# Performance work log

Measured on AMD Instinct MI355X. Metric: run time of the kernel, lower is better.

Reference implementation:

```python
import jax, jax.numpy as jnp
import numpy as np

H = 256; NH = 8; DH = H // NH; L = 2; B = 32; S = 512; FIN = 199; A = 4


def _ln(x, g, b):
    m = jnp.mean(x, -1, keepdims=True)
    v = jnp.mean((x - m) ** 2, -1, keepdims=True)
    return (x - m) / jnp.sqrt(v + 1e-5) * g + b


def _grn(x, fc1w, fc1b, fc2w, fc2b, gw, gb, ggw, ggb, lg, lb):
    # GatedResidualNetwork, input_dim == output_dim so no skip layer, no context
    h = jax.nn.elu(x @ fc1w + fc1b)
    h = jax.nn.elu(h @ fc2w + fc2b)
    g = (h @ gw + gb) * jax.nn.sigmoid(h @ ggw + ggb)  # GLU
    return _ln(g + x, lg, lb)


def _attn(h, wq, bq, wk, bk, wv, bv, wo, bo):
    b, s, _ = h.shape
    q = (h @ wq + bq).reshape(b, s, NH, DH)
    k = (h @ wk + bk).reshape(b, s, NH, DH)
    v = (h @ wv + bv).reshape(b, s, NH, DH)
    scores = jnp.einsum('bqhd,bkhd->bhqk', q, k) / jnp.sqrt(jnp.float32(DH))
    mask = jnp.triu(jnp.ones((s, s), dtype=bool), 1)  # causal: mask strictly-future
    scores = jnp.where(mask, -jnp.inf, scores)
    aw = jax.nn.softmax(scores, axis=-1)
    ctx = jnp.einsum('bhqk,bkhd->bqhd', aw, v).reshape(b, s, H)
    return ctx @ wo + bo, aw


def _pe(s, d):
    pos = jnp.arange(s, dtype=jnp.float32)[:, None]
    div = jnp.exp(jnp.arange(0, d, 2, dtype=jnp.float32) * (-jnp.log(10000.0) / d))
    pe = jnp.zeros((s, d), dtype=jnp.float32)
    pe = pe.at[:, 0::2].set(jnp.sin(pos * div)).at[:, 1::2].set(jnp.cos(pos * div))
    return pe


def setup_inputs():
    key = jax.random.key(0)
    ks = iter(jax.random.split(key, 80))
    def nrm(shape, sc=0.02):
        return (jax.random.normal(next(ks), shape) * sc).astype(jnp.float32)
    d = {}
    d['x'] = jax.random.normal(next(ks), (B, S, FIN), dtype=jnp.float32)
    d['time_features'] = jax.random.normal(next(ks), (B, S, 3), dtype=jnp.float32)
    d['fp_w'] = nrm((FIN, H)); d['fp_b'] = jnp.zeros((H,), jnp.float32)
    d['tp_w'] = nrm((3, H));   d['tp_b'] = jnp.zeros((H,), jnp.float32)
    d['ip_w'] = nrm((H, H));   d['ip_b'] = jnp.zeros((H,), jnp.float32)
    for nm in ['wq', 'wk', 'wv', 'wo']:
        d[nm] = nrm((L, H, H))
    for nm in ['bq', 'bk', 'bv', 'bo']:
        d[nm] = jnp.zeros((L, H), jnp.float32)
    d['ln_g'] = jnp.ones((L, H), jnp.float32); d['ln_b'] = jnp.zeros((L, H), jnp.float32)
    for nm in ['g_fc1w', 'g_fc2w', 'g_gw', 'g_ggw']:
        d[nm] = nrm((L, H, H))
    for nm in ['g_fc1b', 'g_fc2b', 'g_gb', 'g_ggb']:
        d[nm] = jnp.zeros((L, H), jnp.float32)
    d['g_lg'] = jnp.ones((L, H), jnp.float32); d['g_lb'] = jnp.zeros((L, H), jnp.float32)
    for nm in ['f_fc1w', 'f_fc2w', 'f_gw', 'f_ggw']:
        d[nm] = nrm((H, H))
    for nm in ['f_fc1b', 'f_fc2b', 'f_gb', 'f_ggb']:
        d[nm] = jnp.zeros((H,), jnp.float32)
    d['f_lg'] = jnp.ones((H,), jnp.float32); d['f_lb'] = jnp.zeros((H,), jnp.float32)
    d['out_w'] = nrm((H, A)); d['out_b'] = jnp.zeros((A,), jnp.float32)
    return d


def reference(x, time_features, fp_w, fp_b, tp_w, tp_b, ip_w, ip_b,
              wq, bq, wk, bk, wv, bv, wo, bo, ln_g, ln_b,
              g_fc1w, g_fc1b, g_fc2w, g_fc2b, g_gw, g_gb, g_ggw, g_ggb, g_lg, g_lb,
              f_fc1w, f_fc1b, f_fc2w, f_fc2b, f_gw, f_gb, f_ggw, f_ggb, f_lg, f_lb,
              out_w, out_b):
    s = x.shape[1]
    hidden = (x @ fp_w + fp_b) + (time_features @ tp_w + tp_b)
    hidden = hidden @ ip_w + ip_b
    hidden = hidden + _pe(s, H)[None]
    aw = None
    for i in range(L):
        ao, aw = _attn(hidden, wq[i], bq[i], wk[i], bk[i], wv[i], bv[i], wo[i], bo[i])
        hidden = _ln(hidden + ao, ln_g[i], ln_b[i])
        hidden = _grn(hidden, g_fc1w[i], g_fc1b[i], g_fc2w[i], g_fc2b[i],
                      g_gw[i], g_gb[i], g_ggw[i], g_ggb[i], g_lg[i], g_lb[i])
    hidden = _grn(hidden, f_fc1w, f_fc1b, f_fc2w, f_fc2b, f_gw, f_gb, f_ggw, f_ggb, f_lg, f_lb)
    final = hidden[:, -1, :]
    logits = final @ out_w + out_b  # [B, A], one column per target asset
    return (logits, aw)
```

## Files before the change

### kernel.cpp

```cpp
#include <hip/hip_runtime.h>
#include <math.h>
#include <cstddef>

#define H 256
#define NH 8
#define DH 32
#define LAYERS 2
#define BB 32
#define SS 512
#define FINDIM 199
#define AA 4
#define T_TOK (BB*SS)
#define KIN 224

typedef unsigned short u16;
typedef unsigned int u32;
typedef __attribute__((ext_vector_type(8))) short short8;
typedef __attribute__((ext_vector_type(4))) float f4;

__device__ __forceinline__ float b2f(u16 v){
  unsigned u = ((unsigned)v) << 16;
  return __builtin_bit_cast(float, u);
}
__device__ __forceinline__ u16 f2b(float f){
  unsigned u = __builtin_bit_cast(unsigned, f);
  unsigned r = (u + 0x7fffu + ((u >> 16) & 1u)) >> 16;
  return (u16)r;
}
__device__ __forceinline__ float wave_sum(float v){
  #pragma unroll
  for (int mk=1; mk<64; mk<<=1) v += __shfl_xor(v, mk, 64);
  return v;
}

#define GLD_LDS16(g, l) \
  __builtin_amdgcn_global_load_lds((const __attribute__((address_space(1))) void*)(g), \
                                   (__attribute__((address_space(3))) void*)(l), 16, 0, 0)

template<int KC, int WK>
__device__ __forceinline__ void stage_acc(
    const u16* Xl, int sx, const u16* __restrict__ Wt,
    int c0, int l16, int lq, f4 acc[2][2])
{
  #pragma unroll
  for (int mi=0;mi<2;mi++)
    #pragma unroll
    for (int ni=0;ni<2;ni++) acc[mi][ni] = (f4){0.f,0.f,0.f,0.f};
  #pragma unroll
  for (int kc=0;kc<KC;kc++){
    short8 af[2], bf[2];
    af[0] = *(const short8*)&Xl[(l16)*sx      + kc*32 + lq*8];
    af[1] = *(const short8*)&Xl[(16+l16)*sx   + kc*32 + lq*8];
    bf[0] = *(const short8*)(Wt + (size_t)(c0+l16)*WK    + kc*32 + lq*8);
    bf[1] = *(const short8*)(Wt + (size_t)(c0+16+l16)*WK + kc*32 + lq*8);
    #pragma unroll
    for (int mi=0;mi<2;mi++)
      #pragma unroll
      for (int ni=0;ni<2;ni++)
        acc[mi][ni] = __builtin_amdgcn_mfma_f32_16x16x32_bf16(af[mi], bf[ni], acc[mi][ni], 0,0,0);
  }
}

template<int DO_ELU>
__device__ __forceinline__ void stage_store(
    f4 acc[2][2], const float* __restrict__ bias,
    int c0, int l16, int lq, u16* Yl, int sy)
{
  #pragma unroll
  for (int ni=0;ni<2;ni++){
    int col = c0 + ni*16 + l16;
    float bc = bias[col];
    #pragma unroll
    for (int mi=0;mi<2;mi++){
      #pragma unroll
      for (int r=0;r<4;r++){
        int row = mi*16 + lq*4 + r;
        float v = acc[mi][ni][r] + bc;
        if (DO_ELU) v = v > 0.f ? v : expm1f(v);
        Yl[row*sy + col] = f2b(v);
      }
    }
  }
}

__device__ __forceinline__ void tile_load256(const u16* g, u16* Yl, int sy, int t){
  #pragma unroll
  for (int j=0;j<2;j++){
    int u = t + j*512;
    int row = u >> 5, cu = u & 31;
    *(short8*)&Yl[row*sy + cu*8] = *(const short8*)(g + (size_t)row*H + cu*8);
  }
}

__device__ __forceinline__ void tile_ln(
    const u16* Yl, int sy, const float* __restrict__ g, const float* __restrict__ b,
    u16* out, int t)
{
  int w = t >> 6, lane = t & 63;
  #pragma unroll
  for (int rr=0;rr<4;rr++){
    int row = w*4 + rr;
    float xv[4];
    #pragma unroll
    for (int j=0;j<4;j++) xv[j] = b2f(Yl[row*sy + lane*4 + j]);
    float s=0.f, ss=0.f;
    #pragma unroll
    for (int j=0;j<4;j++){ s += xv[j]; ss += xv[j]*xv[j]; }
    s = wave_sum(s); ss = wave_sum(ss);
    float mean = s * (1.0f/H);
    float var  = ss * (1.0f/H) - mean*mean;
    float rstd = rsqrtf(var + 1e-5f);
    ushort4 o;
    int col = lane*4;
    o.x = f2b((xv[0]-mean)*rstd*g[col+0] + b[col+0]);
    o.y = f2b((xv[1]-mean)*rstd*g[col+1] + b[col+1]);
    o.z = f2b((xv[2]-mean)*rstd*g[col+2] + b[col+2]);
    o.w = f2b((xv[3]-mean)*rstd*g[col+3] + b[col+3]);
    *(ushort4*)(out + (size_t)row*H + col) = o;
  }
}

struct WPtrs { const float* p[21]; };

__global__ __launch_bounds__(256) void wconv_kernel(WPtrs wp, u16* __restrict__ dst){
  __shared__ float tl[64][65];
  int mb = blockIdx.x >> 4, tile = blockIdx.x & 15;
  int k0 = (tile >> 2) * 64, n0 = (tile & 3) * 64;
  const float* src = wp.p[mb];
  int t = threadIdx.x;
  int r = t >> 4, cg = t & 15;
  #pragma unroll
  for (int p4=0;p4<4;p4++){
    f4 v = *(const f4*)(src + (size_t)(k0 + r + p4*16)*H + n0 + cg*4);
    tl[r+p4*16][cg*4+0]=v[0]; tl[r+p4*16][cg*4+1]=v[1];
    tl[r+p4*16][cg*4+2]=v[2]; tl[r+p4*16][cg*4+3]=v[3];
  }
  __syncthreads();
  u16* db = dst + (size_t)mb*H*H;
  #pragma unroll
  for (int p4=0;p4<4;p4++){
    int rn = r + p4*16;
    ushort4 o;
    o.x = f2b(tl[cg*4+0][rn]); o.y = f2b(tl[cg*4+1][rn]);
    o.z = f2b(tl[cg*4+2][rn]); o.w = f2b(tl[cg*4+3][rn]);
    *(ushort4*)(db + (size_t)(n0+rn)*H + k0 + cg*4) = o;
  }
}

__global__ __launch_bounds__(256) void wcat_kernel(
    const float* __restrict__ fp_w, const float* __restrict__ tp_w,
    u16* __restrict__ wcat){
  int idx = blockIdx.x*256 + threadIdx.x;
  if (idx >= 256*KIN) return;
  int n = idx / KIN, k2 = idx % KIN;
  float v = 0.f;
  if (k2 < FINDIM) v = fp_w[(size_t)k2*H + n];
  else if (k2 < FINDIM+3) v = tp_w[(size_t)(k2-FINDIM)*H + n];
  wcat[idx] = f2b(v);
}

__global__ __launch_bounds__(256) void xconv_kernel(
    const float* __restrict__ x, const float* __restrict__ tf,
    u16* __restrict__ ab){
  size_t idx = (size_t)blockIdx.x*256 + threadIdx.x;
  if (idx >= (size_t)T_TOK*KIN) return;
  int tok = idx / KIN, k2 = idx % KIN;
  float v = 0.f;
  if (k2 < FINDIM) v = x[(size_t)tok*FINDIM + k2];
  else if (k2 < FINDIM+3) v = tf[(size_t)tok*3 + (k2-FINDIM)];
  ab[idx] = f2b(v);
}

#define SA (KIN+8)
#define SY (H+8)

__global__ __launch_bounds__(512) void input_kernel(
    const u16* __restrict__ ab, const u16* __restrict__ wcat,
    const float* __restrict__ fp_b, const float* __restrict__ tp_b,
    const u16* __restrict__ ipw, const float* __restrict__ ip_b,
    u16* __restrict__ hid){
  __shared__ u16 Al[32*SA];
  __shared__ u16 Tl[32*SY];
  int t = threadIdx.x;
  int tok0 = blockIdx.x * 32;
  int lane = t & 63, w = t >> 6;
  int l16 = lane & 15, lq = lane >> 4;
  int c0 = w * 32;

  #pragma unroll
  for (int j=0;j<2;j++){
    int u = t + j*512;
    if (u < 896){
      int row = u / 28, cu = u % 28;
      *(short8*)&Al[row*SA + cu*8] = *(const short8*)(ab + (size_t)(tok0+row)*KIN + cu*8);
    }
  }
  __syncthreads();

  f4 acc[2][2];
  stage_acc<7, KIN>(Al, SA, wcat, c0, l16, lq, acc);
  #pragma unroll
  for (int ni=0;ni<2;ni++){
    int col = c0 + ni*16 + l16;
    float bc = fp_b[col] + tp_b[col];
    #pragma unroll
    for (int mi=0;mi<2;mi++)
      #pragma unroll
      for (int r=0;r<4;r++){
        int row = mi*16 + lq*4 + r;
        Tl[row*SY + col] = f2b(acc[mi][ni][r] + bc);
      }
  }
  __syncthreads();

  stage_acc<8, H>(Tl, SY, ipw, c0, l16, lq, acc);
  #pragma unroll
  for (int ni=0;ni<2;ni++){
    int col = c0 + ni*16 + l16;
    float bc = ip_b[col];
    int ii = col >> 1;
    float div = __expf((float)(2*ii) * -0.03597789207803197f);
    #pragma unroll
    for (int mi=0;mi<2;mi++)
      #pragma unroll
      for (int r=0;r<4;r++){
        int row = mi*16 + lq*4 + r;
        int s = (tok0 + row) & (SS-1);
        float arg = (float)s * div;
        float pe = (col & 1) ? cosf(arg) : sinf(arg);
        hid[(size_t)(tok0+row)*H + col] = f2b(acc[mi][ni][r] + bc + pe);
      }
  }
}

__global__ __launch_bounds__(512) void oproj_ln_kernel(
    const u16* __restrict__ ctx, u16* __restrict__ hid,
    const u16* __restrict__ wo, const float* __restrict__ bo,
    const float* __restrict__ g, const float* __restrict__ b){
  __shared__ u16 Xl[32*SY];
  __shared__ u16 Rl[32*SY];
  int t = threadIdx.x;
  int tok0 = blockIdx.x * 32;
  int lane = t & 63, w = t >> 6;
  int l16 = lane & 15, lq = lane >> 4;
  int c0 = w * 32;
  u16* hb = hid + (size_t)tok0*H;

  tile_load256(ctx + (size_t)tok0*H, Xl, SY, t);
  tile_load256(hb, Rl, SY, t);
  __syncthreads();

  f4 acc[2][2];
  stage_acc<8, H>(Xl, SY, wo, c0, l16, lq, acc);
  __syncthreads();
  #pragma unroll
  for (int ni=0;ni<2;ni++){
    int col = c0 + ni*16 + l16;
    float bc = bo[col];
    #pragma unroll
    for (int mi=0;mi<2;mi++)
      #pragma unroll
      for (int r=0;r<4;r++){
        int row = mi*16 + lq*4 + r;
        float y = acc[mi][ni][r] + bc + b2f(Rl[row*SY + col]);
        Xl[row*SY + col] = f2b(y);
      }
  }
  __syncthreads();
  tile_ln(Xl, SY, g, b, hb, t);
}

__global__ __launch_bounds__(512) void grn_kernel(
    u16* __restrict__ hid,
    const u16* __restrict__ fc1, const u16* __restrict__ fc2,
    const u16* __restrict__ gw,  const u16* __restrict__ ggw,
    const float* __restrict__ b1, const float* __restrict__ b2,
    const float* __restrict__ gb, const float* __restrict__ ggb,
    const float* __restrict__ lg, const float* __restrict__ lb){
  __shared__ u16 Xl[32*SY];
  __shared__ u16 H1[32*SY];
  __shared__ u16 H2[32*SY];
  int t = threadIdx.x;
  int tok0 = blockIdx.x * 32;
  int lane = t & 63, w = t >> 6;
  int l16 = lane & 15, lq = lane >> 4;
  int c0 = w * 32;
  u16* hb = hid + (size_t)tok0*H;

  tile_load256(hb, Xl, SY, t);
  __syncthreads();

  f4 acc[2][2];
  stage_acc<8, H>(Xl, SY, fc1, c0, l16, lq, acc);
  stage_store<1>(acc, b1, c0, l16, lq, H1, SY);
  __syncthreads();
  stage_acc<8, H>(H1, SY, fc2, c0, l16, lq, acc);
  stage_store<1>(acc, b2, c0, l16, lq, H2, SY);
  __syncthreads();
  stage_acc<8, H>(H2, SY, gw, c0, l16, lq, acc);
  stage_store<0>(acc, gb, c0, l16, lq, H1, SY);
  __syncthreads();
  stage_acc<8, H>(H2, SY, ggw, c0, l16, lq, acc);
  __syncthreads();
  #pragma unroll
  for (int ni=0;ni<2;ni++){
    int col = c0 + ni*16 + l16;
    float bc = ggb[col];
    #pragma unroll
    for (int mi=0;mi<2;mi++)
      #pragma unroll
      for (int r=0;r<4;r++){
        int row = mi*16 + lq*4 + r;
        float gg = acc[mi][ni][r] + bc;
        float sg = 1.0f/(1.0f + __expf(-gg));
        float y  = b2f(H1[row*SY + col]) * sg + b2f(Xl[row*SY + col]);
        H2[row*SY + col] = f2b(y);
      }
  }
  __syncthreads();
  tile_ln(H2, SY, lg, lb, hb, t);
}

struct GemmJob  { const u16* Wt; const float* bias; u16* C; };
struct GemmBatch{ GemmJob j[3]; };

__global__ __launch_bounds__(256) void gemm_bf16(
    const u16* __restrict__ A, GemmBatch jb) {
  __shared__ u16 smem[128*64 + 64*64];
  u16* As  = smem;
  u16* Wsm = smem + 128*64;
  const GemmJob job = jb.j[blockIdx.z];
  const u16* Wt = job.Wt;
  int t = threadIdx.x;
  int m0 = blockIdx.x * 128;
  int n0 = blockIdx.y * 64;
  int lane = t & 63, w = t >> 6;
  int wr = (w >> 1) * 64;
  int wc = (w & 1) * 32;
  int l16 = lane & 15, lq = lane >> 4;

  f4 acc[4][2];
  #pragma unroll
  for (int mi=0;mi<4;mi++)
    #pragma unroll
    for (int ni=0;ni<2;ni++) acc[mi][ni] = (f4){0.f,0.f,0.f,0.f};

  for (int k0=0;k0<256;k0+=64){
    #pragma unroll
    for (int ja=0;ja<4;ja++){
      int ub = (w*4 + ja)*64;
      int u  = ub + lane;
      int m  = u >> 3, c = u & 7, kx = c ^ (m & 7);
      const u16* g = A + (size_t)(m0+m)*H + k0 + kx*8;
      GLD_LDS16(g, As + (size_t)ub*8);
    }
    #pragma unroll
    for (int jb2=0;jb2<2;jb2++){
      int ub = (w*2 + jb2)*64;
      int u  = ub + lane;
      int n  = u >> 3, c = u & 7, kx = c ^ (n & 7);
      const u16* g = Wt + (size_t)(n0+n)*H + k0 + kx*8;
      GLD_LDS16(g, Wsm + (size_t)ub*8);
    }
    __syncthreads();
    #pragma unroll
    for (int kc=0;kc<2;kc++){
      short8 af[4], bf[2];
      int kx = kc*4 + lq;
      #pragma unroll
      for (int mi=0;mi<4;mi++){
        int m = wr + mi*16 + l16;
        int un = (m<<3) | (kx ^ (m&7));
        af[mi] = *(short8*)&As[un*8];
      }
      #pragma unroll
      for (int ni=0;ni<2;ni++){
        int n = wc + ni*16 + l16;
        int un = (n<<3) | (kx ^ (n&7));
        bf[ni] = *(short8*)&Wsm[un*8];
      }
      #pragma unroll
      for (int mi=0;mi<4;mi++)
        #pragma unroll
        for (int ni=0;ni<2;ni++)
          acc[mi][ni] = __builtin_amdgcn_mfma_f32_16x16x32_bf16(af[mi], bf[ni], acc[mi][ni], 0,0,0);
    }
    __syncthreads();
  }

  u16* Cl = smem;
  #pragma unroll
  for (int ni=0;ni<2;ni++){
    int coll = wc + ni*16 + l16;
    float bcol = job.bias[n0 + coll];
    #pragma unroll
    for (int mi=0;mi<4;mi++){
      #pragma unroll
      for (int r=0;r<4;r++){
        int rowl = wr + mi*16 + lq*4 + r;
        Cl[rowl*68 + coll] = f2b(acc[mi][ni][r] + bcol);
      }
    }
  }
  __syncthreads();
  #pragma unroll
  for (int q2=0;q2<4;q2++){
    int u = q2*256 + t;
    int row = u >> 3, cu = u & 7;
    short8 val = *(short8*)&Cl[row*68 + cu*8];
    *(short8*)(job.C + (size_t)(m0+row)*H + n0 + cu*8) = val;
  }
}

template<int WRITE_AW>
__global__ __launch_bounds__(256) void attn_kernel(
    const u16* __restrict__ q, const u16* __restrict__ k,
    const u16* __restrict__ v, float* __restrict__ aw,
    u16* __restrict__ ctx) {
  __shared__ u16 Vt[DH][SS+8];
  __shared__ u16 Plds[4][16][72];
  int t  = threadIdx.x;
  int zg = blockIdx.x;
  int bh = blockIdx.y;
  int b  = bh >> 3, h = bh & 7;
  int lane = t & 63, w = t >> 6;
  int l16 = lane & 15, lq = lane >> 4;
  const float scale = 0.17677669529663687f;

  #pragma unroll
  for (int rep=0;rep<2;rep++){
    int kk = t + rep*256;
    const u16* vp = v + ((size_t)(b*SS + kk))*H + h*DH;
    short8 r0 = *(const short8*)(vp);
    short8 r1 = *(const short8*)(vp+8);
    short8 r2 = *(const short8*)(vp+16);
    short8 r3 = *(const short8*)(vp+24);
    #pragma unroll
    for (int j=0;j<8;j++){
      Vt[j][kk]    = (u16)r0[j];
      Vt[8+j][kk]  = (u16)r1[j];
      Vt[16+j][kk] = (u16)r2[j];
      Vt[24+j][kk] = (u16)r3[j];
    }
  }
  __syncthreads();

  for (int it=0; it<4; it++){
    int qt  = zg + it*2;
    int qr0 = qt*64 + w*16;
    int KT  = qt*4 + w + 1;
    short8 af = *(const short8*)(q + ((size_t)(b*SS + qr0 + l16))*H + h*DH + lq*8);

    float l[4] = {0.f,0.f,0.f,0.f};
    f4 o[2] = {(f4){0.f,0.f,0.f,0.f}, (f4){0.f,0.f,0.f,0.f}};
    u32 pk0[32], pk1[32];

    #pragma unroll
    for (int c8=0;c8<8;c8++){
      if (c8*4 < KT){
        #pragma unroll
        for (int j=0;j<4;j++){
          int kt = c8*4 + j;
          float p[4] = {0.f,0.f,0.f,0.f};
          if (kt < KT){
            short8 bfr = *(const short8*)(k + ((size_t)(b*SS + kt*16 + l16))*H + h*DH + lq*8);
            f4 cc = (f4){0.f,0.f,0.f,0.f};
            cc = __builtin_amdgcn_mfma_f32_16x16x32_bf16(af, bfr, cc, 0,0,0);
            int col = kt*16 + l16;
            #pragma unroll
            for (int i=0;i<4;i++){
              int qi = qr0 + lq*4 + i;
              float sc = (col <= qi) ? cc[i]*scale : -3.0e38f;
              p[i] = __expf(sc);
              l[i] += p[i];
            }
          }
          u16 pb[4];
          #pragma unroll
          for (int i=0;i<4;i++) pb[i] = f2b(p[i]);
          if (WRITE_AW){
            pk0[kt] = (u32)pb[0] | ((u32)pb[1] << 16);
            pk1[kt] = (u32)pb[2] | ((u32)pb[3] << 16);
          }
          #pragma unroll
          for (int i=0;i<4;i++) Plds[w][lq*4+i][j*16+l16] = pb[i];
        }
        #pragma unroll
        for (int kc=0;kc<2;kc++){
          short8 pa = *(short8*)&Plds[w][l16][kc*32 + lq*8];
          #pragma unroll
          for (int dt=0;dt<2;dt++){
            short8 vb = *(const short8*)&Vt[dt*16 + l16][c8*64 + kc*32 + lq*8];
            o[dt] = __builtin_amdgcn_mfma_f32_16x16x32_bf16(pa, vb, o[dt], 0,0,0);
          }
        }
      }
    }

    #pragma unroll
    for (int i=0;i<4;i++){
      #pragma unroll
      for (int mk=1; mk<16; mk<<=1) l[i] += __shfl_xor(l[i], mk, 64);
    }
    float inv[4];
    #pragma unroll
    for (int i=0;i<4;i++) inv[i] = 1.0f / l[i];

    if (WRITE_AW){
      float* ab = aw + (size_t)bh*SS*SS;
      #pragma unroll
      for (int kt=0;kt<32;kt++){
        if (kt < KT){
          int col = kt*16 + l16;
          float pv[4] = { b2f((u16)pk0[kt]), b2f((u16)(pk0[kt]>>16)),
                          b2f((u16)pk1[kt]), b2f((u16)(pk1[kt]>>16)) };
          #pragma unroll
          for (int i=0;i<4;i++){
            int qi = qr0 + lq*4 + i;
            ab[(size_t)qi*SS + col] = (col <= qi) ? pv[i]*inv[i] : 0.f;
          }
        }
      }
      int c4base = KT*4;
      f4 z = (f4){0.f,0.f,0.f,0.f};
      #pragma unroll
      for (int ri=0;ri<4;ri++){
        int row = qr0 + ri*4 + lq;
        for (int j=l16; j < 128 - c4base; j += 16)
          *(f4*)&ab[(size_t)row*SS + (size_t)(c4base+j)*4] = z;
      }
    }

    #pragma unroll
    for (int dt=0;dt<2;dt++){
      #pragma unroll
      for (int i=0;i<4;i++){
        int row = qr0 + lq*4 + i;
        ctx[((size_t)(b*SS + row))*H + h*DH + dt*16 + l16] = f2b(o[dt][i]*inv[i]);
      }
    }
  }
}

__global__ __launch_bounds__(128) void logits_kernel(
    const u16* __restrict__ hid, const float* __restrict__ ow,
    const float* __restrict__ ob, float* __restrict__ out){
  int t = threadIdx.x;
  int b = t >> 2, a = t & 3;
  const u16* hr = hid + ((size_t)b*SS + (SS-1))*H;
  float acc = ob[a];
  for (int k2=0;k2<H;k2++) acc = fmaf(b2f(hr[k2]), ow[k2*AA + a], acc);
  out[t] = acc;
}

extern "C" void kernel_launch(void* const* d_in, const int* in_sizes, int n_in,
                              void* d_out, int out_size, void* d_ws, size_t ws_size,
                              hipStream_t stream){
  (void)in_sizes; (void)n_in; (void)out_size; (void)ws_size;
  const float* x      = (const float*)d_in[0];
  const float* tf     = (const float*)d_in[1];
  const float* fp_w   = (const float*)d_in[2];
  const float* fp_b   = (const float*)d_in[3];
  const float* tp_w   = (const float*)d_in[4];
  const float* tp_b   = (const float*)d_in[5];
  const float* ip_w   = (const float*)d_in[6];
  const float* ip_b   = (const float*)d_in[7];
  const float* wq     = (const float*)d_in[8];
  const float* wk     = (const float*)d_in[9];
  const float* wv     = (const float*)d_in[10];
  const float* wo     = (const float*)d_in[11];
  const float* bq     = (const float*)d_in[12];
  const float* bk     = (const float*)d_in[13];
  const float* bv     = (const float*)d_in[14];
  const float* bo     = (const float*)d_in[15];
  const float* ln_g   = (const float*)d_in[16];
  const float* ln_b   = (const float*)d_in[17];
  const float* g_fc1w = (const float*)d_in[18];
  const float* g_fc2w = (const float*)d_in[19];
  const float* g_gw   = (const float*)d_in[20];
  const float* g_ggw  = (const float*)d_in[21];
  const float* g_fc1b = (const float*)d_in[22];
  const float* g_fc2b = (const float*)d_in[23];
  const float* g_gb   = (const float*)d_in[24];
  const float* g_ggb  = (const float*)d_in[25];
  const float* g_lg   = (const float*)d_in[26];
  const float* g_lb   = (const float*)d_in[27];
  const float* f_fc1w = (const float*)d_in[28];
  const float* f_fc2w = (const float*)d_in[29];
  const float* f_gw   = (const float*)d_in[30];
  const float* f_ggw  = (const float*)d_in[31];
  const float* f_fc1b = (const float*)d_in[32];
  const float* f_fc2b = (const float*)d_in[33];
  const float* f_gb   = (const float*)d_in[34];
  const float* f_ggb  = (const float*)d_in[35];
  const float* f_lg   = (const float*)d_in[36];
  const float* f_lb   = (const float*)d_in[37];
  const float* out_w  = (const float*)d_in[38];
  const float* out_b  = (const float*)d_in[39];

  float* logits = (float*)d_out;
  float* aw     = logits + BB*AA;

  u16* wts = (u16*)d_ws;
  const size_t WMAT = (size_t)H*H;
  u16* wcat = wts  + 21*WMAT;
  u16* abuf = wcat + (size_t)H*KIN;
  u16* hid  = abuf + (size_t)T_TOK*KIN;
  size_t BUF = (size_t)T_TOK * H;
  u16* buf1 = hid  + BUF;
  u16* buf2 = buf1 + BUF;
  u16* buf3 = buf2 + BUF;

  WPtrs wp;
  wp.p[0]  = ip_w;
  wp.p[1]  = wq;        wp.p[2]  = wq + WMAT;
  wp.p[3]  = wk;        wp.p[4]  = wk + WMAT;
  wp.p[5]  = wv;        wp.p[6]  = wv + WMAT;
  wp.p[7]  = wo;        wp.p[8]  = wo + WMAT;
  wp.p[9]  = g_fc1w;    wp.p[10] = g_fc1w + WMAT;
  wp.p[11] = g_fc2w;    wp.p[12] = g_fc2w + WMAT;
  wp.p[13] = g_gw;      wp.p[14] = g_gw + WMAT;
  wp.p[15] = g_ggw;     wp.p[16] = g_ggw + WMAT;
  wp.p[17] = f_fc1w;    wp.p[18] = f_fc2w;
  wp.p[19] = f_gw;      wp.p[20] = f_ggw;
  const int WT_IP=0, WT_Q=1, WT_K=3, WT_V=5, WT_O=7,
            WT_FC1=9, WT_FC2=11, WT_GW=13, WT_GGW=15,
            WT_FFC1=17, WT_FFC2=18, WT_FGW=19, WT_FGGW=20;

  dim3 b256(256), b512(512);
  dim3 gAttn(2, BB*NH);
  dim3 gTok(T_TOK/32);

  wconv_kernel<<<21*16, b256, 0, stream>>>(wp, wts);
  wcat_kernel<<<(H*KIN+255)/256, b256, 0, stream>>>(fp_w, tp_w, wcat);
  xconv_kernel<<<(T_TOK*KIN+255)/256, b256, 0, stream>>>(x, tf, abuf);
  input_kernel<<<gTok, b512, 0, stream>>>(abuf, wcat, fp_b, tp_b,
                                          wts + (size_t)WT_IP*WMAT, ip_b, hid);

  for (int i=0;i<LAYERS;i++){
    const size_t BOFF = (size_t)i*H;
    GemmBatch gb;
    gb.j[0] = { wts + (size_t)(WT_Q+i)*WMAT, bq+BOFF, buf1 };
    gb.j[1] = { wts + (size_t)(WT_K+i)*WMAT, bk+BOFF, buf2 };
    gb.j[2] = { wts + (size_t)(WT_V+i)*WMAT, bv+BOFF, buf3 };
    gemm_bf16<<<dim3(T_TOK/128, H/64, 3), b256, 0, stream>>>(hid, gb);
    if (i == LAYERS-1)
      attn_kernel<1><<<gAttn, b256, 0, stream>>>(buf1, buf2, buf3, aw, buf1);
    else
      attn_kernel<0><<<gAttn, b256, 0, stream>>>(buf1, buf2, buf3, aw, buf1);
    oproj_ln_kernel<<<gTok, b512, 0, stream>>>(buf1, hid,
        wts + (size_t)(WT_O+i)*WMAT, bo+BOFF, ln_g+BOFF, ln_b+BOFF);
    grn_kernel<<<gTok, b512, 0, stream>>>(hid,
        wts + (size_t)(WT_FC1+i)*WMAT, wts + (size_t)(WT_FC2+i)*WMAT,
        wts + (size_t)(WT_GW+i)*WMAT,  wts + (size_t)(WT_GGW+i)*WMAT,
        g_fc1b+BOFF, g_fc2b+BOFF, g_gb+BOFF, g_ggb+BOFF,
        g_lg+BOFF, g_lb+BOFF);
  }

  grn_kernel<<<gTok, b512, 0, stream>>>(hid,
      wts + (size_t)WT_FFC1*WMAT, wts + (size_t)WT_FFC2*WMAT,
      wts + (size_t)WT_FGW*WMAT,  wts + (size_t)WT_FGGW*WMAT,
      f_fc1b, f_fc2b, f_gb, f_ggb, f_lg, f_lb);

  logits_kernel<<<1, 128, 0, stream>>>(hid, out_w, out_b, logits);
}
```

Before: 673.8 us.

## Use 64-token tiles in row-wise kernels and fuse logits into final GRN

Doubles the token tile in the input, o-proj+LN and GRN kernels to 64 rows, with each wave computing a 32x64 output block, so each weight fragment loaded from global memory feeds twice as many MFMAs. Shared memory is cut by reading residuals straight from global and holding the sigmoid gate in registers as packed fp16. The logits projection is folded into the last GRN kernel, and attention-weight stores become nontemporal. The trade-offs are higher register pressure with fewer blocks, and a small precision change from the fp16 gate.

```diff
diff --git a/kernel.cpp b/kernel.cpp
--- a/kernel.cpp
+++ b/kernel.cpp
@@ -1,4 +1,5 @@
 #include <hip/hip_runtime.h>
+#include <hip/hip_fp16.h>
 #include <math.h>
 #include <cstddef>
 
@@ -12,6 +13,7 @@
 #define AA 4
 #define T_TOK (BB*SS)
 #define KIN 224
+#define TPB 64
 
 typedef unsigned short u16;
 typedef unsigned int u32;
@@ -37,44 +39,49 @@
   __builtin_amdgcn_global_load_lds((const __attribute__((address_space(1))) void*)(g), \
                                    (__attribute__((address_space(3))) void*)(l), 16, 0, 0)
 
+#define SA (KIN+8)
+#define SY (H+8)
+
 template<int KC, int WK>
-__device__ __forceinline__ void stage_acc(
+__device__ __forceinline__ void stage_acc64(
     const u16* Xl, int sx, const u16* __restrict__ Wt,
-    int c0, int l16, int lq, f4 acc[2][2])
+    int r0, int c0, int l16, int lq, f4 acc[2][4])
 {
   #pragma unroll
   for (int mi=0;mi<2;mi++)
     #pragma unroll
-    for (int ni=0;ni<2;ni++) acc[mi][ni] = (f4){0.f,0.f,0.f,0.f};
+    for (int ni=0;ni<4;ni++) acc[mi][ni] = (f4){0.f,0.f,0.f,0.f};
   #pragma unroll
   for (int kc=0;kc<KC;kc++){
-    short8 af[2], bf[2];
-    af[0] = *(const short8*)&Xl[(l16)*sx      + kc*32 + lq*8];
-    af[1] = *(const short8*)&Xl[(16+l16)*sx   + kc*32 + lq*8];
-    bf[0] = *(const short8*)(Wt + (size_t)(c0+l16)*WK    + kc*32 + lq*8);
-    bf[1] = *(const short8*)(Wt + (size_t)(c0+16+l16)*WK + kc*32 + lq*8);
+    short8 af[2], bf[4];
     #pragma unroll
     for (int mi=0;mi<2;mi++)
-      #pragma unroll
-      for (int ni=0;ni<2;ni++)
+      af[mi] = *(const short8*)&Xl[(r0 + mi*16 + l16)*sx + kc*32 + lq*8];
+    #pragma unroll
+    for (int ni=0;ni<4;ni++)
+      bf[ni] = *(const short8*)(Wt + (size_t)(c0 + ni*16 + l16)*WK + kc*32 + lq*8);
+    #pragma unroll
+    for (int mi=0;mi<2;mi++)
+      #pragma unroll
+      for (int ni=0;ni<4;ni++)
         acc[mi][ni] = __builtin_amdgcn_mfma_f32_16x16x32_bf16(af[mi], bf[ni], acc[mi][ni], 0,0,0);
   }
 }
 
 template<int DO_ELU>
-__device__ __forceinline__ void stage_store(
-    f4 acc[2][2], const float* __restrict__ bias,
-    int c0, int l16, int lq, u16* Yl, int sy)
+__device__ __forceinline__ void stage_store64(
+    f4 acc[2][4], const float* __restrict__ bias,
+    int r0, int c0, int l16, int lq, u16* Yl, int sy)
 {
   #pragma unroll
-  for (int ni=0;ni<2;ni++){
+  for (int ni=0;ni<4;ni++){
     int col = c0 + ni*16 + l16;
     float bc = bias[col];
     #pragma unroll
     for (int mi=0;mi<2;mi++){
       #pragma unroll
       for (int r=0;r<4;r++){
-        int row = mi*16 + lq*4 + r;
+        int row = r0 + mi*16 + lq*4 + r;
         float v = acc[mi][ni][r] + bc;
         if (DO_ELU) v = v > 0.f ? v : expm1f(v);
         Yl[row*sy + col] = f2b(v);
@@ -83,23 +90,24 @@
   }
 }
 
-__device__ __forceinline__ void tile_load256(const u16* g, u16* Yl, int sy, int t){
-  #pragma unroll
-  for (int j=0;j<2;j++){
+__device__ __forceinline__ void tile_load64(const u16* g, u16* Yl, int sy, int t){
+  #pragma unroll
+  for (int j=0;j<4;j++){
     int u = t + j*512;
     int row = u >> 5, cu = u & 31;
     *(short8*)&Yl[row*sy + cu*8] = *(const short8*)(g + (size_t)row*H + cu*8);
   }
 }
 
-__device__ __forceinline__ void tile_ln(
-    const u16* Yl, int sy, const float* __restrict__ g, const float* __restrict__ b,
+template<int WB>
+__device__ __forceinline__ void tile_ln64(
+    u16* Yl, int sy, const float* __restrict__ g, const float* __restrict__ b,
     u16* out, int t)
 {
   int w = t >> 6, lane = t & 63;
   #pragma unroll
-  for (int rr=0;rr<4;rr++){
-    int row = w*4 + rr;
+  for (int rr=0;rr<8;rr++){
+    int row = w*8 + rr;
     float xv[4];
     #pragma unroll
     for (int j=0;j<4;j++) xv[j] = b2f(Yl[row*sy + lane*4 + j]);
@@ -117,6 +125,7 @@
     o.z = f2b((xv[2]-mean)*rstd*g[col+2] + b[col+2]);
     o.w = f2b((xv[3]-mean)*rstd*g[col+3] + b[col+3]);
     *(ushort4*)(out + (size_t)row*H + col) = o;
+    if (WB && row == 63) *(ushort4*)(Yl + row*sy + col) = o;
   }
 }
 
@@ -171,51 +180,49 @@
   ab[idx] = f2b(v);
 }
 
-#define SA (KIN+8)
-#define SY (H+8)
-
-__global__ __launch_bounds__(512) void input_kernel(
+__global__ __launch_bounds__(512,4) void input_kernel(
     const u16* __restrict__ ab, const u16* __restrict__ wcat,
     const float* __restrict__ fp_b, const float* __restrict__ tp_b,
     const u16* __restrict__ ipw, const float* __restrict__ ip_b,
     u16* __restrict__ hid){
-  __shared__ u16 Al[32*SA];
-  __shared__ u16 Tl[32*SY];
+  __shared__ u16 Al[TPB*SA];
+  __shared__ u16 Tl[TPB*SY];
   int t = threadIdx.x;
-  int tok0 = blockIdx.x * 32;
+  int tok0 = blockIdx.x * TPB;
   int lane = t & 63, w = t >> 6;
   int l16 = lane & 15, lq = lane >> 4;
-  int c0 = w * 32;
-
-  #pragma unroll
-  for (int j=0;j<2;j++){
+  int r0 = (w >> 2) * 32;
+  int c0 = (w & 3) * 64;
+
+  #pragma unroll
+  for (int j=0;j<4;j++){
     int u = t + j*512;
-    if (u < 896){
+    if (u < 1792){
       int row = u / 28, cu = u % 28;
       *(short8*)&Al[row*SA + cu*8] = *(const short8*)(ab + (size_t)(tok0+row)*KIN + cu*8);
     }
   }
   __syncthreads();
 
-  f4 acc[2][2];
-  stage_acc<7, KIN>(Al, SA, wcat, c0, l16, lq, acc);
-  #pragma unroll
-  for (int ni=0;ni<2;ni++){
+  f4 acc[2][4];
+  stage_acc64<7, KIN>(Al, SA, wcat, r0, c0, l16, lq, acc);
+  #pragma unroll
+  for (int ni=0;ni<4;ni++){
     int col = c0 + ni*16 + l16;
     float bc = fp_b[col] + tp_b[col];
     #pragma unroll
     for (int mi=0;mi<2;mi++)
       #pragma unroll
       for (int r=0;r<4;r++){
-        int row = mi*16 + lq*4 + r;
+        int row = r0 + mi*16 + lq*4 + r;
         Tl[row*SY + col] = f2b(acc[mi][ni][r] + bc);
       }
   }
   __syncthreads();
 
-  stage_acc<8, H>(Tl, SY, ipw, c0, l16, lq, acc);
-  #pragma unroll
-  for (int ni=0;ni<2;ni++){
+  stage_acc64<8, H>(Tl, SY, ipw, r0, c0, l16, lq, acc);
+  #pragma unroll
+  for (int ni=0;ni<4;ni++){
     int col = c0 + ni*16 + l16;
     float bc = ip_b[col];
     int ii = col >> 1;
@@ -224,7 +231,7 @@
     for (int mi=0;mi<2;mi++)
       #pragma unroll
       for (int r=0;r<4;r++){
-        int row = mi*16 + lq*4 + r;
+        int row = r0 + mi*16 + lq*4 + r;
         int s = (tok0 + row) & (SS-1);
         float arg = (float)s * div;
         float pe = (col & 1) ? cosf(arg) : sinf(arg);
@@ -233,92 +240,136 @@
   }
 }
 
-__global__ __launch_bounds__(512) void oproj_ln_kernel(
+__global__ __launch_bounds__(512,4) void oproj_ln_kernel(
     const u16* __restrict__ ctx, u16* __restrict__ hid,
     const u16* __restrict__ wo, const float* __restrict__ bo,
     const float* __restrict__ g, const float* __restrict__ b){
-  __shared__ u16 Xl[32*SY];
-  __shared__ u16 Rl[32*SY];
+  __shared__ u16 Xl[TPB*SY];
   int t = threadIdx.x;
-  int tok0 = blockIdx.x * 32;
+  int tok0 = blockIdx.x * TPB;
   int lane = t & 63, w = t >> 6;
   int l16 = lane & 15, lq = lane >> 4;
-  int c0 = w * 32;
+  int r0 = (w >> 2) * 32;
+  int c0 = (w & 3) * 64;
   u16* hb = hid + (size_t)tok0*H;
 
-  tile_load256(ctx + (size_t)tok0*H, Xl, SY, t);
-  tile_load256(hb, Rl, SY, t);
-  __syncthreads();
-
-  f4 acc[2][2];
-  stage_acc<8, H>(Xl, SY, wo, c0, l16, lq, acc);
-  __syncthreads();
-  #pragma unroll
-  for (int ni=0;ni<2;ni++){
+  tile_load64(ctx + (size_t)tok0*H, Xl, SY, t);
+  __syncthreads();
+
+  f4 acc[2][4];
+  stage_acc64<8, H>(Xl, SY, wo, r0, c0, l16, lq, acc);
+  __syncthreads();
+  #pragma unroll
+  for (int ni=0;ni<4;ni++){
     int col = c0 + ni*16 + l16;
     float bc = bo[col];
     #pragma unroll
     for (int mi=0;mi<2;mi++)
       #pragma unroll
       for (int r=0;r<4;r++){
-        int row = mi*16 + lq*4 + r;
-        float y = acc[mi][ni][r] + bc + b2f(Rl[row*SY + col]);
+        int row = r0 + mi*16 + lq*4 + r;
+        float y = acc[mi][ni][r] + bc + b2f(hb[(size_t)row*H + col]);
         Xl[row*SY + col] = f2b(y);
       }
   }
   __syncthreads();
-  tile_ln(Xl, SY, g, b, hb, t);
-}
-
-__global__ __launch_bounds__(512) void grn_kernel(
+  tile_ln64<0>(Xl, SY, g, b, hb, t);
+}
+
+template<int LOGITS>
+__global__ __launch_bounds__(512,4) void grn_kernel(
     u16* __restrict__ hid,
     const u16* __restrict__ fc1, const u16* __restrict__ fc2,
     const u16* __restrict__ gw,  const u16* __restrict__ ggw,
     const float* __restrict__ b1, const float* __restrict__ b2,
     const float* __restrict__ gb, const float* __restrict__ ggb,
-    const float* __restrict__ lg, const float* __restrict__ lb){
-  __shared__ u16 Xl[32*SY];
-  __shared__ u16 H1[32*SY];
-  __shared__ u16 H2[32*SY];
+    const float* __restrict__ lg, const float* __restrict__ lb,
+    const float* __restrict__ ow, const float* __restrict__ ob,
+    float* __restrict__ lout){
+  __shared__ u16 Xa[TPB*SY];
+  __shared__ u16 Xb[TPB*SY];
   int t = threadIdx.x;
-  int tok0 = blockIdx.x * 32;
+  int tok0 = blockIdx.x * TPB;
   int lane = t & 63, w = t >> 6;
   int l16 = lane & 15, lq = lane >> 4;
-  int c0 = w * 32;
+  int r0 = (w >> 2) * 32;
+  int c0 = (w & 3) * 64;
   u16* hb = hid + (size_t)tok0*H;
 
-  tile_load256(hb, Xl, SY, t);
-  __syncthreads();
-
-  f4 acc[2][2];
-  stage_acc<8, H>(Xl, SY, fc1, c0, l16, lq, acc);
-  stage_store<1>(acc, b1, c0, l16, lq, H1, SY);
-  __syncthreads();
-  stage_acc<8, H>(H1, SY, fc2, c0, l16, lq, acc);
-  stage_store<1>(acc, b2, c0, l16, lq, H2, SY);
-  __syncthreads();
-  stage_acc<8, H>(H2, SY, gw, c0, l16, lq, acc);
-  stage_store<0>(acc, gb, c0, l16, lq, H1, SY);
-  __syncthreads();
-  stage_acc<8, H>(H2, SY, ggw, c0, l16, lq, acc);
-  __syncthreads();
-  #pragma unroll
-  for (int ni=0;ni<2;ni++){
+  tile_load64(hb, Xa, SY, t);
+  __syncthreads();
+
+  f4 acc[2][4];
+  stage_acc64<8, H>(Xa, SY, fc1, r0, c0, l16, lq, acc);
+  stage_store64<1>(acc, b1, r0, c0, l16, lq, Xb, SY);
+  __syncthreads();
+  stage_acc64<8, H>(Xb, SY, fc2, r0, c0, l16, lq, acc);
+  stage_store64<1>(acc, b2, r0, c0, l16, lq, Xa, SY);
+  __syncthreads();
+
+  stage_acc64<8, H>(Xa, SY, ggw, r0, c0, l16, lq, acc);
+  u32 sgp[2][4][2];
+  #pragma unroll
+  for (int mi=0;mi<2;mi++)
+    #pragma unroll
+    for (int ni=0;ni<4;ni++){
+      float bc = ggb[c0 + ni*16 + l16];
+      float s0 = 1.0f/(1.0f + __expf(-(acc[mi][ni][0]+bc)));
+      float s1 = 1.0f/(1.0f + __expf(-(acc[mi][ni][1]+bc)));
+      float s2 = 1.0f/(1.0f + __expf(-(acc[mi][ni][2]+bc)));
+      float s3 = 1.0f/(1.0f + __expf(-(acc[mi][ni][3]+bc)));
+      sgp[mi][ni][0] = __builtin_bit_cast(u32, __floats2half2_rn(s0, s1));
+      sgp[mi][ni][1] = __builtin_bit_cast(u32, __floats2half2_rn(s2, s3));
+    }
+
+  stage_acc64<8, H>(Xa, SY, gw, r0, c0, l16, lq, acc);
+  #pragma unroll
+  for (int ni=0;ni<4;ni++){
     int col = c0 + ni*16 + l16;
-    float bc = ggb[col];
-    #pragma unroll
-    for (int mi=0;mi<2;mi++)
+    float bc = gb[col];
+    #pragma unroll
+    for (int mi=0;mi<2;mi++){
+      float2 s01 = __half22float2(__builtin_bit_cast(__half2, sgp[mi][ni][0]));
+      float2 s23 = __half22float2(__builtin_bit_cast(__half2, sgp[mi][ni][1]));
+      float sv[4] = {s01.x, s01.y, s23.x, s23.y};
       #pragma unroll
       for (int r=0;r<4;r++){
-        int row = mi*16 + lq*4 + r;
-        float gg = acc[mi][ni][r] + bc;
-        float sg = 1.0f/(1.0f + __expf(-gg));
-        float y  = b2f(H1[row*SY + col]) * sg + b2f(Xl[row*SY + col]);
-        H2[row*SY + col] = f2b(y);
-      }
-  }
-  __syncthreads();
-  tile_ln(H2, SY, lg, lb, hb, t);
+        int row = r0 + mi*16 + lq*4 + r;
+        float y = (acc[mi][ni][r] + bc) * sv[r] + b2f(hb[(size_t)row*H + col]);
+        Xb[row*SY + col] = f2b(y);
+      }
+    }
+  }
+  __syncthreads();
+  tile_ln64<LOGITS>(Xb, SY, lg, lb, hb, t);
+
+  if (LOGITS){
+    if ((tok0 & (SS-1)) == SS - TPB){
+      __syncthreads();
+      if (t < 64){
+        int bidx = tok0 >> 9;
+        float a0=0.f, a1=0.f, a2=0.f, a3=0.f;
+        #pragma unroll
+        for (int j=0;j<4;j++){
+          int k = t*4 + j;
+          float xv = b2f(Xb[63*SY + k]);
+          f4 wr = *(const f4*)(ow + (size_t)k*AA);
+          a0 = fmaf(xv, wr[0], a0);
+          a1 = fmaf(xv, wr[1], a1);
+          a2 = fmaf(xv, wr[2], a2);
+          a3 = fmaf(xv, wr[3], a3);
+        }
+        a0 = wave_sum(a0); a1 = wave_sum(a1);
+        a2 = wave_sum(a2); a3 = wave_sum(a3);
+        if (t == 0){
+          lout[bidx*AA+0] = a0 + ob[0];
+          lout[bidx*AA+1] = a1 + ob[1];
+          lout[bidx*AA+2] = a2 + ob[2];
+          lout[bidx*AA+3] = a3 + ob[3];
+        }
+      }
+    }
+  }
 }
 
 struct GemmJob  { const u16* Wt; const float* bias; u16* C; };
@@ -517,7 +568,8 @@
           #pragma unroll
           for (int i=0;i<4;i++){
             int qi = qr0 + lq*4 + i;
-            ab[(size_t)qi*SS + col] = (col <= qi) ? pv[i]*inv[i] : 0.f;
+            float val = (col <= qi) ? pv[i]*inv[i] : 0.f;
+            __builtin_nontemporal_store(val, &ab[(size_t)qi*SS + col]);
           }
         }
       }
@@ -527,7 +579,7 @@
       for (int ri=0;ri<4;ri++){
         int row = qr0 + ri*4 + lq;
         for (int j=l16; j < 128 - c4base; j += 16)
-          *(f4*)&ab[(size_t)row*SS + (size_t)(c4base+j)*4] = z;
+          __builtin_nontemporal_store(z, (f4*)&ab[(size_t)row*SS + (size_t)(c4base+j)*4]);
       }
     }
 
@@ -540,17 +592,6 @@
       }
     }
   }
-}
-
-__global__ __launch_bounds__(128) void logits_kernel(
-    const u16* __restrict__ hid, const float* __restrict__ ow,
-    const float* __restrict__ ob, float* __restrict__ out){
-  int t = threadIdx.x;
-  int b = t >> 2, a = t & 3;
-  const u16* hr = hid + ((size_t)b*SS + (SS-1))*H;
-  float acc = ob[a];
-  for (int k2=0;k2<H;k2++) acc = fmaf(b2f(hr[k2]), ow[k2*AA + a], acc);
-  out[t] = acc;
 }
 
 extern "C" void kernel_launch(void* const* d_in, const int* in_sizes, int n_in,
@@ -629,7 +670,7 @@
 
   dim3 b256(256), b512(512);
   dim3 gAttn(2, BB*NH);
-  dim3 gTok(T_TOK/32);
+  dim3 gTok(T_TOK/TPB);
 
   wconv_kernel<<<21*16, b256, 0, stream>>>(wp, wts);
   wcat_kernel<<<(H*KIN+255)/256, b256, 0, stream>>>(fp_w, tp_w, wcat);
@@ -650,17 +691,16 @@
       attn_kernel<0><<<gAttn, b256, 0, stream>>>(buf1, buf2, buf3, aw, buf1);
     oproj_ln_kernel<<<gTok, b512, 0, stream>>>(buf1, hid,
         wts + (size_t)(WT_O+i)*WMAT, bo+BOFF, ln_g+BOFF, ln_b+BOFF);
-    grn_kernel<<<gTok, b512, 0, stream>>>(hid,
+    grn_kernel<0><<<gTok, b512, 0, stream>>>(hid,
         wts + (size_t)(WT_FC1+i)*WMAT, wts + (size_t)(WT_FC2+i)*WMAT,
         wts + (size_t)(WT_GW+i)*WMAT,  wts + (size_t)(WT_GGW+i)*WMAT,
         g_fc1b+BOFF, g_fc2b+BOFF, g_gb+BOFF, g_ggb+BOFF,
-        g_lg+BOFF, g_lb+BOFF);
-  }
-
-  grn_kernel<<<gTok, b512, 0, stream>>>(hid,
+        g_lg+BOFF, g_lb+BOFF, nullptr, nullptr, nullptr);
+  }
+
+  grn_kernel<1><<<gTok, b512, 0, stream>>>(hid,
       wts + (size_t)WT_FFC1*WMAT, wts + (size_t)WT_FFC2*WMAT,
       wts + (size_t)WT_FGW*WMAT,  wts + (size_t)WT_FGGW*WMAT,
-      f_fc1b, f_fc2b, f_gb, f_ggb, f_lg, f_lb);
-
-  logits_kernel<<<1, 128, 0, stream>>>(hid, out_w, out_b, logits);
-}
+      f_fc1b, f_fc2b, f_gb, f_ggb, f_lg, f_lb,
+      out_w, out_b, logits);
+}
```

Result: slower. 688.3 us (+2.2%).
